# Kernel optimization log

Hardware: AMD Instinct MI355X
Metric: run time of the kernel (lower is better)

## Reference

```python
import jax, jax.numpy as jnp
import numpy as np

B, N, E, C1, C2 = 8, 4096, 2048, 128, 128
DENSITY = 0.05  # incidence matrix sparsity (stored dense, as in the original)


def setup_inputs() -> dict:
    key = jax.random.key(0)
    kx, kh, kw = jax.random.split(key, 3)
    x = jax.random.normal(kx, (B, N, C1), dtype=jnp.float32)
    # binary hypergraph incidence matrix [B, n_node, n_edge]
    H = (jax.random.uniform(kh, (B, N, E)) < DENSITY).astype(jnp.float32)
    W = jax.random.normal(kw, (C1, C2), dtype=jnp.float32) * 0.02
    b = jnp.zeros((C2,), dtype=jnp.float32)
    return {"x": x, "H": H, "W": W, "b": b}


def _mean_agg(path, X):
    # path: [B, T, S], X: [B, S, D] -> mean-aggregated [B, T, D]
    out = jnp.matmul(path, X)
    s = jnp.sum(path, axis=2, keepdims=True)  # [B, T, 1]
    # 1/s with inf (s==0) masked to 0, fused as a single where
    return jnp.where(s > 0, out / s, jnp.zeros_like(out))


def reference(x, H, W, b):
    # fc: [B, N, C1] -> [B, N, C2]
    x = jnp.matmul(x, W) + b
    # v2e: aggregate node features into hyperedge features
    Ht = jnp.swapaxes(H, 1, 2)  # [B, E, N]
    e = _mean_agg(Ht, x)        # [B, E, C2]
    # e2v: aggregate hyperedge features back to nodes
    v = _mean_agg(H, e)         # [B, N, C2]
    return v
```

## Files before the change

kernel.cpp:

```cpp
#include <hip/hip_runtime.h>
#include <stdint.h>

constexpr int B_ = 8, N_ = 4096, E_ = 2048, C_ = 128;
constexpr int CN = 144;
constexpr int KT = 32;
constexpr int MT = 32;
constexpr int NWK = 4;
constexpr int LRF = 145;

typedef short bf16x8 __attribute__((ext_vector_type(8)));
typedef float f32x4  __attribute__((ext_vector_type(4)));

__device__ inline uint16_t bf16_rne(float f) {
    uint32_t u = __builtin_bit_cast(uint32_t, f);
    return (uint16_t)((u + 0x7FFFu + ((u >> 16) & 1u)) >> 16);
}

constexpr size_t HT_E  = (size_t)B_ * (N_ / 32) * E_;
constexpr size_t WT_E  = (size_t)CN * C_;
constexpr size_t EBF_E = (size_t)B_ * CN * E_;

__global__ void pack_kernel(const float* __restrict__ H, uint32_t* __restrict__ HT) {
    const int t  = threadIdx.x;
    const int eg = blockIdx.x & 7;
    const int ng = (blockIdx.x >> 3) & 127;
    const int b  = blockIdx.x >> 10;
    const int e  = eg * 256 + t;
    const float* hp = H + ((size_t)b * N_ + ng * 32) * E_ + e;
    uint32_t w = 0;
#pragma unroll
    for (int i = 0; i < 32; ++i) w |= (hp[(size_t)i * E_] > 0.5f) ? (1u << i) : 0u;
    HT[((size_t)b * (N_ / 32) + ng) * E_ + e] = w;
}

__global__ void prep_kernel(const float* __restrict__ W, uint16_t* __restrict__ WTb,
                            uint32_t* __restrict__ xwbT32, uint32_t* __restrict__ ebfT32) {
    const int NW = (int)WT_E;
    const int NX = B_ * 16 * (N_ / 2);
    const int NE = B_ * 16 * (E_ / 2);
    int stride = gridDim.x * blockDim.x;
    for (int i = blockIdx.x * blockDim.x + threadIdx.x; i < NW + NX + NE; i += stride) {
        if (i < NW) {
            int c = i >> 7, k = i & 127;
            WTb[i] = bf16_rne((c < C_) ? W[k * C_ + c] : 0.f);
        } else if (i < NW + NX) {
            int j = i - NW;
            int b = j >> 15, rr = j & 32767;
            int r = rr >> 11, n2 = rr & 2047;
            xwbT32[((size_t)b * CN + (C_ + r)) * (N_ / 2) + n2] = (r == 0) ? 0x3F803F80u : 0u;
        } else {
            int j = i - NW - NX;
            int b = j >> 14, rr = j & 16383;
            int r = rr >> 10, e2 = rr & 1023;
            ebfT32[((size_t)b * CN + (C_ + r)) * (E_ / 2) + e2] = (r == 0) ? 0x3F803F80u : 0u;
        }
    }
}

template <int MODE>
__global__ __launch_bounds__(256, 2)
void gemm_k(const float* __restrict__ Ax, const uint32_t* __restrict__ HT,
            const uint16_t* __restrict__ Btb, const float* __restrict__ bias,
            uint16_t* __restrict__ outT, float* __restrict__ outF) {
    constexpr int K  = (MODE == 0) ? C_ : (MODE == 1) ? N_ : E_;
    constexpr int KW = K / NWK;
    constexpr int SW = KW / KT;
    constexpr size_t BBS = (MODE == 0) ? 0 : (size_t)CN * K;
    constexpr int OLD = (MODE == 0) ? N_ : E_;

    __shared__ float R[2 * 32 * LRF];

    const int t = threadIdx.x, wave = t >> 6, lane = t & 63;
    const int l15 = lane & 15, quad = lane >> 4;
    const int batch = blockIdx.x & 7;
    const int m0 = (blockIdx.x >> 3) * MT;
    const int kw = wave * KW;

    const uint16_t* Bp = Btb + (size_t)batch * BBS;
    const uint32_t* Hp = HT + (size_t)batch * (N_ / 32) * E_;

    f32x4 acc[18];
#pragma unroll
    for (int i = 0; i < 18; ++i) acc[i] = (f32x4){0.f, 0.f, 0.f, 0.f};

    float    af0[16], af1[16];
    uint32_t aw0[2], aw1_[2];
    uint4    ax0[2], ax1[2];
    bf16x8   bf0[9], bf1[9];

    auto loadA = [&](int k0, int buf) __attribute__((always_inline)) {
        if constexpr (MODE == 0) {
            float* dst = buf ? af1 : af0;
#pragma unroll
            for (int g = 0; g < 2; ++g) {
                const float* ap = Ax + ((size_t)batch * N_ + m0 + g * 16 + l15) * C_ + k0 + quad * 8;
                const float4 f0 = *(const float4*)ap;
                const float4 f1 = *(const float4*)(ap + 4);
                dst[g * 8 + 0] = f0.x; dst[g * 8 + 1] = f0.y; dst[g * 8 + 2] = f0.z; dst[g * 8 + 3] = f0.w;
                dst[g * 8 + 4] = f1.x; dst[g * 8 + 5] = f1.y; dst[g * 8 + 6] = f1.z; dst[g * 8 + 7] = f1.w;
            }
        } else if constexpr (MODE == 1) {
            uint32_t* dst = buf ? aw1_ : aw0;
            const uint32_t* p = Hp + (size_t)(k0 >> 5) * E_ + m0 + l15;
            dst[0] = p[0];
            dst[1] = p[16];
        } else {
            uint4* dst = buf ? ax1 : ax0;
            const uint32_t* p = Hp + (size_t)(m0 >> 5) * E_ + k0 + quad * 8;
            dst[0] = *(const uint4*)p;
            dst[1] = *(const uint4*)(p + 4);
        }
    };
    auto loadB = [&](int k0, int buf) __attribute__((always_inline)) {
        bf16x8* dst = buf ? bf1 : bf0;
#pragma unroll
        for (int j = 0; j < 9; ++j)
            dst[j] = *(const bf16x8*)&Bp[(size_t)(j * 16 + l15) * K + k0 + quad * 8];
    };
    auto compute = [&](int buf) __attribute__((always_inline)) {
        bf16x8 a0, a1;
        if constexpr (MODE == 0) {
            const float* src = buf ? af1 : af0;
#pragma unroll
            for (int jj = 0; jj < 8; ++jj) {
                a0[jj] = (short)bf16_rne(src[jj]);
                a1[jj] = (short)bf16_rne(src[8 + jj]);
            }
        } else if constexpr (MODE == 1) {
            const uint32_t* src = buf ? aw1_ : aw0;
            const int base = quad * 8;
#pragma unroll
            for (int jj = 0; jj < 8; ++jj) {
                a0[jj] = (short)(((src[0] >> (base + jj)) & 1u) ? 0x3F80 : 0);
                a1[jj] = (short)(((src[1] >> (base + jj)) & 1u) ? 0x3F80 : 0);
            }
        } else {
            const uint4* src = buf ? ax1 : ax0;
            const uint32_t u[8] = {src[0].x, src[0].y, src[0].z, src[0].w,
                                   src[1].x, src[1].y, src[1].z, src[1].w};
#pragma unroll
            for (int jj = 0; jj < 8; ++jj) {
                a0[jj] = (short)(((u[jj] >> l15) & 1u) ? 0x3F80 : 0);
                a1[jj] = (short)(((u[jj] >> (16 + l15)) & 1u) ? 0x3F80 : 0);
            }
        }
        const bf16x8* bsrc = buf ? bf1 : bf0;
#pragma unroll
        for (int j = 0; j < 9; ++j) {
            acc[j]     = __builtin_amdgcn_mfma_f32_16x16x32_bf16(a0, bsrc[j], acc[j],     0, 0, 0);
            acc[9 + j] = __builtin_amdgcn_mfma_f32_16x16x32_bf16(a1, bsrc[j], acc[9 + j], 0, 0, 0);
        }
    };

    loadA(kw, 0); loadB(kw, 0);
#pragma unroll 1
    for (int s = 0; s < SW; s += 2) {
        if (s + 1 < SW) { loadA(kw + (s + 1) * KT, 1); loadB(kw + (s + 1) * KT, 1); }
        compute(0);
        if (s + 1 < SW) {
            if (s + 2 < SW) { loadA(kw + (s + 2) * KT, 0); loadB(kw + (s + 2) * KT, 0); }
            compute(1);
        }
    }

    auto stR = [&](int base) __attribute__((always_inline)) {
#pragma unroll
        for (int g = 0; g < 2; ++g)
#pragma unroll
            for (int j = 0; j < 9; ++j)
#pragma unroll
                for (int r = 0; r < 4; ++r)
                    R[base + (g * 16 + quad * 4 + r) * LRF + j * 16 + l15] = acc[g * 9 + j][r];
    };
    auto ldR = [&](int base) __attribute__((always_inline)) {
#pragma unroll
        for (int g = 0; g < 2; ++g)
#pragma unroll
            for (int j = 0; j < 9; ++j)
#pragma unroll
                for (int r = 0; r < 4; ++r)
                    acc[g * 9 + j][r] += R[base + (g * 16 + quad * 4 + r) * LRF + j * 16 + l15];
    };
    if (wave == 1) stR(0);
    if (wave == 3) stR(32 * LRF);
    __syncthreads();
    if (wave == 0) ldR(0);
    if (wave == 2) ldR(32 * LRF);
    __syncthreads();
    if (wave == 2) stR(0);
    __syncthreads();
    if (wave != 0) return;
    ldR(0);

    float mul[2][4];
    if constexpr (MODE != 0) {
#pragma unroll
        for (int g = 0; g < 2; ++g)
#pragma unroll
            for (int r = 0; r < 4; ++r) {
                float sv = __shfl(acc[g * 9 + 8][r], lane & 48);
                mul[g][r] = (sv > 0.f) ? 1.f / sv : 0.f;
            }
    }
#pragma unroll
    for (int g = 0; g < 2; ++g) {
        const int row = m0 + g * 16 + quad * 4;
        if constexpr (MODE == 2) {
            float* op = outF + ((size_t)batch * N_ + row) * C_;
#pragma unroll
            for (int j = 0; j < 8; ++j) {
                int c = j * 16 + l15;
#pragma unroll
                for (int r = 0; r < 4; ++r) op[(size_t)r * C_ + c] = acc[g * 9 + j][r] * mul[g][r];
            }
        } else {
#pragma unroll
            for (int j = 0; j < 8; ++j) {
                int c = j * 16 + l15;
                float v0, v1, v2, v3;
                if constexpr (MODE == 0) {
                    float bb = bias[c];
                    v0 = acc[g * 9 + j][0] + bb; v1 = acc[g * 9 + j][1] + bb;
                    v2 = acc[g * 9 + j][2] + bb; v3 = acc[g * 9 + j][3] + bb;
                } else {
                    v0 = acc[g * 9 + j][0] * mul[g][0]; v1 = acc[g * 9 + j][1] * mul[g][1];
                    v2 = acc[g * 9 + j][2] * mul[g][2]; v3 = acc[g * 9 + j][3] * mul[g][3];
                }
                uint32_t q0 = (uint32_t)bf16_rne(v0) | ((uint32_t)bf16_rne(v1) << 16);
                uint32_t q1 = (uint32_t)bf16_rne(v2) | ((uint32_t)bf16_rne(v3) << 16);
                uint16_t* op = outT + ((size_t)batch * CN + c) * OLD + row;
                *(uint2*)op = make_uint2(q0, q1);
            }
        }
    }
}

extern "C" void kernel_launch(void* const* d_in, const int* in_sizes, int n_in,
                              void* d_out, int out_size, void* d_ws, size_t ws_size,
                              hipStream_t stream) {
    const float* x    = (const float*)d_in[0];
    const float* H    = (const float*)d_in[1];
    const float* W    = (const float*)d_in[2];
    const float* bias = (const float*)d_in[3];
    float* out = (float*)d_out;

    uint32_t* HT   = (uint32_t*)d_ws;
    uint16_t* WTb  = (uint16_t*)(HT + HT_E);
    uint16_t* ebfT = WTb + WT_E;
    uint16_t* xwbT = (uint16_t*)d_out;

    pack_kernel<<<dim3(8192), dim3(256), 0, stream>>>(H, HT);
    prep_kernel<<<dim3(1024), dim3(256), 0, stream>>>(W, WTb, (uint32_t*)xwbT, (uint32_t*)ebfT);
    gemm_k<0><<<dim3(8 * (N_ / MT)), dim3(256), 0, stream>>>(x, nullptr, WTb, bias, xwbT, nullptr);
    gemm_k<1><<<dim3(8 * (E_ / MT)), dim3(256), 0, stream>>>(nullptr, HT, xwbT, nullptr, ebfT, nullptr);
    gemm_k<2><<<dim3(8 * (N_ / MT)), dim3(256), 0, stream>>>(nullptr, HT, ebfT, nullptr, nullptr, out);
}
```

Measured before the change: 524.2 us.

## Fuse pack, prep and three GEMM stages into one cooperative kernel

Replaces the five separate launches (H bit-packing, weight/ones-row prep, and three GEMM stages) with one cooperative kernel. The stages are separated by grid-wide syncs, and each 512-thread block runs two 256-thread GEMM tiles side by side. The aim is to remove launch gaps and tail effects between the stages. In exchange, the grid is fixed at 256 blocks, so the memory-bound H packing has fewer threads in flight. The tighter launch bounds also halve the per-thread register budget, which could cause spills in the MFMA accumulator-heavy GEMM.

```diff
diff --git a/kernel.cpp b/kernel.cpp
--- a/kernel.cpp
+++ b/kernel.cpp
@@ -1,5 +1,8 @@
 #include <hip/hip_runtime.h>
+#include <hip/hip_cooperative_groups.h>
 #include <stdint.h>
+
+namespace cg = cooperative_groups;
 
 constexpr int B_ = 8, N_ = 4096, E_ = 2048, C_ = 128;
 constexpr int CN = 144;
@@ -7,6 +10,7 @@
 constexpr int MT = 32;
 constexpr int NWK = 4;
 constexpr int LRF = 145;
+constexpr int GR  = 2 * 32 * LRF;
 
 typedef short bf16x8 __attribute__((ext_vector_type(8)));
 typedef float f32x4  __attribute__((ext_vector_type(4)));
@@ -20,64 +24,26 @@
 constexpr size_t WT_E  = (size_t)CN * C_;
 constexpr size_t EBF_E = (size_t)B_ * CN * E_;
 
-__global__ void pack_kernel(const float* __restrict__ H, uint32_t* __restrict__ HT) {
-    const int t  = threadIdx.x;
-    const int eg = blockIdx.x & 7;
-    const int ng = (blockIdx.x >> 3) & 127;
-    const int b  = blockIdx.x >> 10;
-    const int e  = eg * 256 + t;
-    const float* hp = H + ((size_t)b * N_ + ng * 32) * E_ + e;
-    uint32_t w = 0;
-#pragma unroll
-    for (int i = 0; i < 32; ++i) w |= (hp[(size_t)i * E_] > 0.5f) ? (1u << i) : 0u;
-    HT[((size_t)b * (N_ / 32) + ng) * E_ + e] = w;
-}
-
-__global__ void prep_kernel(const float* __restrict__ W, uint16_t* __restrict__ WTb,
-                            uint32_t* __restrict__ xwbT32, uint32_t* __restrict__ ebfT32) {
-    const int NW = (int)WT_E;
-    const int NX = B_ * 16 * (N_ / 2);
-    const int NE = B_ * 16 * (E_ / 2);
-    int stride = gridDim.x * blockDim.x;
-    for (int i = blockIdx.x * blockDim.x + threadIdx.x; i < NW + NX + NE; i += stride) {
-        if (i < NW) {
-            int c = i >> 7, k = i & 127;
-            WTb[i] = bf16_rne((c < C_) ? W[k * C_ + c] : 0.f);
-        } else if (i < NW + NX) {
-            int j = i - NW;
-            int b = j >> 15, rr = j & 32767;
-            int r = rr >> 11, n2 = rr & 2047;
-            xwbT32[((size_t)b * CN + (C_ + r)) * (N_ / 2) + n2] = (r == 0) ? 0x3F803F80u : 0u;
-        } else {
-            int j = i - NW - NX;
-            int b = j >> 14, rr = j & 16383;
-            int r = rr >> 10, e2 = rr & 1023;
-            ebfT32[((size_t)b * CN + (C_ + r)) * (E_ / 2) + e2] = (r == 0) ? 0x3F803F80u : 0u;
-        }
-    }
-}
-
 template <int MODE>
-__global__ __launch_bounds__(256, 2)
-void gemm_k(const float* __restrict__ Ax, const uint32_t* __restrict__ HT,
-            const uint16_t* __restrict__ Btb, const float* __restrict__ bias,
-            uint16_t* __restrict__ outT, float* __restrict__ outF) {
+__device__ __forceinline__ void gemm_block(
+        int vb, int tg, float* __restrict__ R,
+        const float* __restrict__ Ax, const uint32_t* __restrict__ HTp,
+        const uint16_t* __restrict__ Btb, const float* __restrict__ bias,
+        uint16_t* __restrict__ outT, float* __restrict__ outF) {
     constexpr int K  = (MODE == 0) ? C_ : (MODE == 1) ? N_ : E_;
     constexpr int KW = K / NWK;
     constexpr int SW = KW / KT;
     constexpr size_t BBS = (MODE == 0) ? 0 : (size_t)CN * K;
     constexpr int OLD = (MODE == 0) ? N_ : E_;
 
-    __shared__ float R[2 * 32 * LRF];
-
-    const int t = threadIdx.x, wave = t >> 6, lane = t & 63;
+    const int wave = tg >> 6, lane = tg & 63;
     const int l15 = lane & 15, quad = lane >> 4;
-    const int batch = blockIdx.x & 7;
-    const int m0 = (blockIdx.x >> 3) * MT;
-    const int kw = wave * KW;
+    const int batch = vb & 7;
+    const int m0 = (vb >> 3) * MT;
+    const int kwv = wave * KW;
 
     const uint16_t* Bp = Btb + (size_t)batch * BBS;
-    const uint32_t* Hp = HT + (size_t)batch * (N_ / 32) * E_;
+    const uint32_t* Hp = HTp + (size_t)batch * (N_ / 32) * E_;
 
     f32x4 acc[18];
 #pragma unroll
@@ -152,13 +118,13 @@
         }
     };
 
-    loadA(kw, 0); loadB(kw, 0);
+    loadA(kwv, 0); loadB(kwv, 0);
 #pragma unroll 1
     for (int s = 0; s < SW; s += 2) {
-        if (s + 1 < SW) { loadA(kw + (s + 1) * KT, 1); loadB(kw + (s + 1) * KT, 1); }
+        if (s + 1 < SW) { loadA(kwv + (s + 1) * KT, 1); loadB(kwv + (s + 1) * KT, 1); }
         compute(0);
         if (s + 1 < SW) {
-            if (s + 2 < SW) { loadA(kw + (s + 2) * KT, 0); loadB(kw + (s + 2) * KT, 0); }
+            if (s + 2 < SW) { loadA(kwv + (s + 2) * KT, 0); loadB(kwv + (s + 2) * KT, 0); }
             compute(1);
         }
     }
@@ -189,50 +155,119 @@
     __syncthreads();
     if (wave == 2) stR(0);
     __syncthreads();
-    if (wave != 0) return;
-    ldR(0);
-
-    float mul[2][4];
-    if constexpr (MODE != 0) {
-#pragma unroll
-        for (int g = 0; g < 2; ++g)
-#pragma unroll
-            for (int r = 0; r < 4; ++r) {
-                float sv = __shfl(acc[g * 9 + 8][r], lane & 48);
-                mul[g][r] = (sv > 0.f) ? 1.f / sv : 0.f;
-            }
+
+    if (wave == 0) {
+        ldR(0);
+        float mul[2][4];
+        if constexpr (MODE != 0) {
+#pragma unroll
+            for (int g = 0; g < 2; ++g)
+#pragma unroll
+                for (int r = 0; r < 4; ++r) {
+                    float sv = __shfl(acc[g * 9 + 8][r], lane & 48);
+                    mul[g][r] = (sv > 0.f) ? 1.f / sv : 0.f;
+                }
+        }
+#pragma unroll
+        for (int g = 0; g < 2; ++g) {
+            const int row = m0 + g * 16 + quad * 4;
+            if constexpr (MODE == 2) {
+                float* op = outF + ((size_t)batch * N_ + row) * C_;
+#pragma unroll
+                for (int j = 0; j < 8; ++j) {
+                    int c = j * 16 + l15;
+#pragma unroll
+                    for (int r = 0; r < 4; ++r) op[(size_t)r * C_ + c] = acc[g * 9 + j][r] * mul[g][r];
+                }
+            } else {
+#pragma unroll
+                for (int j = 0; j < 8; ++j) {
+                    int c = j * 16 + l15;
+                    float v0, v1, v2, v3;
+                    if constexpr (MODE == 0) {
+                        float bb = bias[c];
+                        v0 = acc[g * 9 + j][0] + bb; v1 = acc[g * 9 + j][1] + bb;
+                        v2 = acc[g * 9 + j][2] + bb; v3 = acc[g * 9 + j][3] + bb;
+                    } else {
+                        v0 = acc[g * 9 + j][0] * mul[g][0]; v1 = acc[g * 9 + j][1] * mul[g][1];
+                        v2 = acc[g * 9 + j][2] * mul[g][2]; v3 = acc[g * 9 + j][3] * mul[g][3];
+                    }
+                    uint32_t q0 = (uint32_t)bf16_rne(v0) | ((uint32_t)bf16_rne(v1) << 16);
+                    uint32_t q1 = (uint32_t)bf16_rne(v2) | ((uint32_t)bf16_rne(v3) << 16);
+                    uint16_t* op = outT + ((size_t)batch * CN + c) * OLD + row;
+                    *(uint2*)op = make_uint2(q0, q1);
+                }
+            }
+        }
     }
-#pragma unroll
-    for (int g = 0; g < 2; ++g) {
-        const int row = m0 + g * 16 + quad * 4;
-        if constexpr (MODE == 2) {
-            float* op = outF + ((size_t)batch * N_ + row) * C_;
-#pragma unroll
-            for (int j = 0; j < 8; ++j) {
-                int c = j * 16 + l15;
-#pragma unroll
-                for (int r = 0; r < 4; ++r) op[(size_t)r * C_ + c] = acc[g * 9 + j][r] * mul[g][r];
-            }
-        } else {
-#pragma unroll
-            for (int j = 0; j < 8; ++j) {
-                int c = j * 16 + l15;
-                float v0, v1, v2, v3;
-                if constexpr (MODE == 0) {
-                    float bb = bias[c];
-                    v0 = acc[g * 9 + j][0] + bb; v1 = acc[g * 9 + j][1] + bb;
-                    v2 = acc[g * 9 + j][2] + bb; v3 = acc[g * 9 + j][3] + bb;
-                } else {
-                    v0 = acc[g * 9 + j][0] * mul[g][0]; v1 = acc[g * 9 + j][1] * mul[g][1];
-                    v2 = acc[g * 9 + j][2] * mul[g][2]; v3 = acc[g * 9 + j][3] * mul[g][3];
-                }
-                uint32_t q0 = (uint32_t)bf16_rne(v0) | ((uint32_t)bf16_rne(v1) << 16);
-                uint32_t q1 = (uint32_t)bf16_rne(v2) | ((uint32_t)bf16_rne(v3) << 16);
-                uint16_t* op = outT + ((size_t)batch * CN + c) * OLD + row;
-                *(uint2*)op = make_uint2(q0, q1);
+    __syncthreads();
+}
+
+__global__ __launch_bounds__(512, 2)
+void fused_k(const float* __restrict__ x, const float* __restrict__ H,
+             const float* __restrict__ W, const float* __restrict__ bias,
+             float* __restrict__ out, uint32_t* __restrict__ HT,
+             uint16_t* __restrict__ WTb, uint16_t* __restrict__ ebfT) {
+    __shared__ float R[2 * GR];
+    cg::grid_group grid = cg::this_grid();
+    const int g  = threadIdx.x >> 8;
+    const int tg = threadIdx.x & 255;
+    uint16_t* xwbT = (uint16_t*)out;
+
+    {
+        const int nth = gridDim.x * blockDim.x;
+        const int tid = blockIdx.x * blockDim.x + threadIdx.x;
+        for (int w = tid; w < (int)HT_E; w += nth) {
+            const int e  = w & (E_ - 1);
+            const int ng = (w >> 11) & 127;
+            const int b  = w >> 18;
+            const float* hp = H + ((size_t)b * N_ + ng * 32) * E_ + e;
+            uint32_t v = 0;
+#pragma unroll
+            for (int i = 0; i < 32; ++i) v |= (hp[(size_t)i * E_] > 0.5f) ? (1u << i) : 0u;
+            HT[w] = v;
+        }
+        const int NW = (int)WT_E;
+        const int NX = B_ * 16 * (N_ / 2);
+        const int NE = B_ * 16 * (E_ / 2);
+        uint32_t* xw32 = (uint32_t*)xwbT;
+        uint32_t* eb32 = (uint32_t*)ebfT;
+        for (int i = tid; i < NW + NX + NE; i += nth) {
+            if (i < NW) {
+                int c = i >> 7, k = i & 127;
+                WTb[i] = bf16_rne((c < C_) ? W[k * C_ + c] : 0.f);
+            } else if (i < NW + NX) {
+                int j = i - NW;
+                int b = j >> 15, rr = j & 32767;
+                int r = rr >> 11, n2 = rr & 2047;
+                xw32[((size_t)b * CN + (C_ + r)) * (N_ / 2) + n2] = (r == 0) ? 0x3F803F80u : 0u;
+            } else {
+                int j = i - NW - NX;
+                int b = j >> 14, rr = j & 16383;
+                int r = rr >> 10, e2 = rr & 1023;
+                eb32[((size_t)b * CN + (C_ + r)) * (E_ / 2) + e2] = (r == 0) ? 0x3F803F80u : 0u;
             }
         }
     }
+    __threadfence();
+    grid.sync();
+
+#pragma unroll 1
+    for (int it = 0; it < 2; ++it)
+        gemm_block<0>(blockIdx.x * 2 + g + it * 512, tg, R + g * GR,
+                      x, nullptr, WTb, bias, xwbT, nullptr);
+    __threadfence();
+    grid.sync();
+
+    gemm_block<1>(blockIdx.x * 2 + g, tg, R + g * GR,
+                  nullptr, HT, xwbT, nullptr, ebfT, nullptr);
+    __threadfence();
+    grid.sync();
+
+#pragma unroll 1
+    for (int it = 0; it < 2; ++it)
+        gemm_block<2>(blockIdx.x * 2 + g + it * 512, tg, R + g * GR,
+                      nullptr, HT, ebfT, nullptr, nullptr, out);
 }
 
 extern "C" void kernel_launch(void* const* d_in, const int* in_sizes, int n_in,
@@ -247,11 +282,8 @@
     uint32_t* HT   = (uint32_t*)d_ws;
     uint16_t* WTb  = (uint16_t*)(HT + HT_E);
     uint16_t* ebfT = WTb + WT_E;
-    uint16_t* xwbT = (uint16_t*)d_out;
-
-    pack_kernel<<<dim3(8192), dim3(256), 0, stream>>>(H, HT);
-    prep_kernel<<<dim3(1024), dim3(256), 0, stream>>>(W, WTb, (uint32_t*)xwbT, (uint32_t*)ebfT);
-    gemm_k<0><<<dim3(8 * (N_ / MT)), dim3(256), 0, stream>>>(x, nullptr, WTb, bias, xwbT, nullptr);
-    gemm_k<1><<<dim3(8 * (E_ / MT)), dim3(256), 0, stream>>>(nullptr, HT, xwbT, nullptr, ebfT, nullptr);
-    gemm_k<2><<<dim3(8 * (N_ / MT)), dim3(256), 0, stream>>>(nullptr, HT, ebfT, nullptr, nullptr, out);
-}
+
+    void* args[8] = {(void*)&x, (void*)&H, (void*)&W, (void*)&bias,
+                     (void*)&out, (void*)&HT, (void*)&WTb, (void*)&ebfT};
+    hipLaunchCooperativeKernel((void*)fused_k, dim3(256), dim3(512), args, 0, stream);
+}
```

After: 812.5 us. +55.0%, slower.
